# Performance work log

Hardware: AMD Instinct MI355X
Metric: run time of the kernel (lower is better)

The kernel has to match this reference:

```python
import jax, jax.numpy as jnp
import numpy as np

B, N, H, E, P = 2, 20000, 128, 200000, 3


def _mlp2(x, w1, b1, w2, b2):
    # Linear -> SiLU -> Linear
    return jax.nn.silu(x @ w1 + b1) @ w2 + b2


def setup_inputs() -> dict:
    key = jax.random.key(0)
    ks = iter(jax.random.split(key, 40))
    def nrm(shape, s=0.05):
        return jax.random.normal(next(ks), shape, dtype=jnp.float32) * s
    inp = {
        "features": jax.random.normal(next(ks), (B, N, H), dtype=jnp.float32),
        "positions": jax.random.normal(next(ks), (B, N, P), dtype=jnp.float32),
        "edge_index_up": jax.random.randint(next(ks), (2, E), 0, N, dtype=jnp.int32),
        "edge_index_down": jax.random.randint(next(ks), (2, E), 0, N, dtype=jnp.int32),
        "degree_up": jax.random.uniform(next(ks), (N,), minval=1.0, maxval=32.0, dtype=jnp.float32),
        "degree_down": jax.random.uniform(next(ks), (N,), minval=1.0, maxval=32.0, dtype=jnp.float32),
    }
    for name in ("up", "down"):
        inp[f"w_msg1_{name}"] = nrm((2 * H + 1, H)); inp[f"b_msg1_{name}"] = jnp.zeros((H,), jnp.float32)
        inp[f"w_msg2_{name}"] = nrm((H, H));         inp[f"b_msg2_{name}"] = jnp.zeros((H,), jnp.float32)
        inp[f"w_pos1_{name}"] = nrm((H, H));         inp[f"b_pos1_{name}"] = jnp.zeros((H,), jnp.float32)
        inp[f"w_pos2_{name}"] = nrm((H, 1));         inp[f"b_pos2_{name}"] = jnp.zeros((1,), jnp.float32)
    inp["w_upd1"] = nrm((2 * H, H)); inp["b_upd1"] = jnp.zeros((H,), jnp.float32)
    inp["w_upd2"] = nrm((H, H));     inp["b_upd2"] = jnp.zeros((H,), jnp.float32)
    return inp


def reference(features, positions, edge_index_up, edge_index_down, degree_up, degree_down,
              w_msg1_up, b_msg1_up, w_msg2_up, b_msg2_up,
              w_pos1_up, b_pos1_up, w_pos2_up, b_pos2_up,
              w_msg1_down, b_msg1_down, w_msg2_down, b_msg2_down,
              w_pos1_down, b_pos1_down, w_pos2_down, b_pos2_down,
              w_upd1, b_upd1, w_upd2, b_upd2):
    n_neighborhoods = 2
    msg_acc = jnp.zeros_like(features)
    pos_upd = jnp.zeros_like(positions)
    neighborhoods = [
        (edge_index_up, degree_up,
         (w_msg1_up, b_msg1_up, w_msg2_up, b_msg2_up),
         (w_pos1_up, b_pos1_up, w_pos2_up, b_pos2_up)),
        (edge_index_down, degree_down,
         (w_msg1_down, b_msg1_down, w_msg2_down, b_msg2_down),
         (w_pos1_down, b_pos1_down, w_pos2_down, b_pos2_down)),
    ]
    for edge_index, degree, msg_p, pos_p in neighborhoods:
        src, dst = edge_index[0], edge_index[1]
        h_src = features[:, src, :]                     # [B, E, H] gather
        h_dst = features[:, dst, :]                     # [B, E, H] gather
        rel_pos = positions[:, src, :] - positions[:, dst, :]  # [B, E, P]
        dist = jnp.linalg.norm(rel_pos, axis=-1, keepdims=True)  # [B, E, 1]
        msg_input = jnp.concatenate([h_src, h_dst, dist], axis=-1)  # [B, E, 2H+1]
        messages = _mlp2(msg_input, *msg_p)             # [B, E, H]
        agg = jnp.zeros_like(features).at[:, dst, :].add(messages)  # scatter-add over dim 1
        agg = agg / jnp.clip(degree, 1.0, None)[None, :, None]
        msg_acc = msg_acc + agg
        weights = jnp.tanh(_mlp2(messages, *pos_p))     # [B, E, 1]
        pos_upd = pos_upd + jnp.zeros_like(positions).at[:, dst, :].add(weights * rel_pos)
    feat_update = _mlp2(jnp.concatenate([features, msg_acc], axis=-1), w_upd1, b_upd1, w_upd2, b_upd2)
    updated_features = features + feat_update
    updated_positions = positions + pos_upd / n_neighborhoods
    return updated_features, updated_positions
```

## Files before the change

kernel.cpp:

```cpp
#include <hip/hip_runtime.h>

#define BB 2
#define NN 20000
#define HH 128
#define EE 200000
#define EBLK 3125
#define NBLK 79

typedef unsigned short u16;
typedef __attribute__((ext_vector_type(4))) float f32x4;
typedef __bf16 bf16x8 __attribute__((ext_vector_type(8)));

#define MFMA(a, b, c) __builtin_amdgcn_mfma_f32_16x16x32_bf16((a), (b), (c), 0, 0, 0)

__device__ __forceinline__ float bf2f(u16 u) {
    union { unsigned int i; float f; } v; v.i = ((unsigned int)u) << 16; return v.f;
}
__device__ __forceinline__ u16 f2bf(float f) {
    union { __bf16 h; u16 u; } v; v.h = (__bf16)f; return v.u;
}
__device__ __forceinline__ float silu_f(float z) { return z / (1.f + __expf(-z)); }

__global__ void detect_kernel(const u16* __restrict__ f, int* __restrict__ flag) {
    int tid = threadIdx.x;
    u16 v = f[tid * 2];
    int e = (v >> 7) & 0xFF;
    int ok = (e >= 101 && e <= 143) ? 1 : 0;
    __shared__ int cnt;
    if (tid == 0) cnt = 0;
    __syncthreads();
    atomicAdd(&cnt, ok);
    __syncthreads();
    if (tid == 0) *flag = (cnt < 200) ? 1 : 0;
}

#define CTOT 5461776
struct P24 { const void* p[24]; };

__global__ __launch_bounds__(256) void canon_kernel(P24 ptrs, const int* __restrict__ flag,
                                                    u16* __restrict__ canon) {
    static const int off[25] = {
        0, 5120000, 5240000, 5260000, 5280000, 5312896, 5313024, 5329408,
        5329536, 5345920, 5346048, 5346176, 5346184, 5379080, 5379208, 5395592,
        5395720, 5412104, 5412232, 5412360, 5412368, 5445136, 5445264, 5461648,
        5461776 };
    static const int rsz[24] = {
        5120000, 120000, 20000, 20000,
        32896, 128, 16384, 128, 16384, 128, 128, 1,
        32896, 128, 16384, 128, 16384, 128, 128, 1,
        32768, 128, 16384, 128 };
    int i = blockIdx.x * 256 + threadIdx.x;
    if (i >= CTOT) return;
    int t = 0;
#pragma unroll 1
    while (i >= off[t + 1]) ++t;
    int j = i - off[t];
    u16 v;
    if (j >= rsz[t]) v = 0;
    else if (*flag) v = f2bf(((const float*)ptrs.p[t])[j]);
    else v = ((const u16*)ptrs.p[t])[j];
    canon[i] = v;
}

__global__ void make_frag(const u16* __restrict__ W, u16* __restrict__ F) {
    int tid = blockIdx.x * 256 + threadIdx.x;
    int j = tid & 7, lane = (tid >> 3) & 63, nt = (tid >> 9) & 7, kt = tid >> 12;
    int k = kt * 32 + ((lane >> 4) * 8) + j;
    int n = nt * 16 + (lane & 15);
    F[tid] = W[k * 128 + n];
}

__global__ void count2_kernel(const int* __restrict__ eu, const int* __restrict__ ed,
                              int* __restrict__ cu, int* __restrict__ cd) {
    int e = blockIdx.x * 256 + threadIdx.x;
    if (e < EE) atomicAdd(&cu[eu[EE + e]], 1);
    else { e -= EE; if (e < EE) atomicAdd(&cd[ed[EE + e]], 1); }
}

struct SP { const int* cnt[2]; int* cur[2]; int* bsum[2]; };

__global__ __launch_bounds__(256) void scan1_kernel(SP p) {
    int half = blockIdx.x / NBLK;
    int b = blockIdx.x - half * NBLK;
    int t = threadIdx.x;
    int i = b * 256 + t;
    __shared__ int buf[256];
    int v = (i < NN) ? p.cnt[half][i] : 0;
    buf[t] = v;
    __syncthreads();
    for (int s = 1; s < 256; s <<= 1) {
        int x = (t >= s) ? buf[t - s] : 0;
        __syncthreads();
        buf[t] += x;
        __syncthreads();
    }
    if (i < NN) p.cur[half][i] = buf[t] - v;
    if (t == 255) p.bsum[half][b] = buf[255];
}

__global__ __launch_bounds__(256) void scan2_kernel(int* __restrict__ bu, int* __restrict__ bd) {
    __shared__ int buf[2][128];
    int half = threadIdx.x >> 7, t = threadIdx.x & 127;
    int* bs = half ? bd : bu;
    int v = (t < NBLK) ? bs[t] : 0;
    buf[half][t] = v;
    __syncthreads();
    for (int s = 1; s < 128; s <<= 1) {
        int x = (t >= s) ? buf[half][t - s] : 0;
        __syncthreads();
        buf[half][t] += x;
        __syncthreads();
    }
    if (t < NBLK) bs[t] = buf[half][t] - v;
}

__global__ void scan3_kernel(int* __restrict__ cu, const int* __restrict__ bu,
                             int* __restrict__ cd, const int* __restrict__ bd) {
    int i = blockIdx.x * 256 + threadIdx.x;
    if (i < NN) cu[i] += bu[i >> 8];
    else { i -= NN; if (i < NN) cd[i] += bd[i >> 8]; }
}

__global__ void scatter2_kernel(const int* __restrict__ eu, const int* __restrict__ ed,
                                int* __restrict__ cu, int* __restrict__ cd,
                                int* __restrict__ su, int* __restrict__ sd) {
    int e = blockIdx.x * 256 + threadIdx.x;
    if (e < EE) { int p = atomicAdd(&cu[eu[EE + e]], 1); su[p] = e; }
    else { e -= EE; if (e < EE) { int p = atomicAdd(&cd[ed[EE + e]], 1); sd[p] = e; } }
}

struct EP {
    const int* eidx; const int* es; const u16* deg;
    const u16* fW1; const u16* w1last; const u16* bias1;
    const u16* fW2; const u16* bias2;
    const u16* fP1; const u16* biasp1;
    const u16* wp2; const u16* biasp2;
};

__global__ __launch_bounds__(256, 4) void edge_kernel(
    const u16* __restrict__ feat, const u16* __restrict__ posit,
    EP up, EP dn,
    float* __restrict__ msg_acc, float* __restrict__ pos_acc)
{
    const int tid = threadIdx.x;
    const int lane = tid & 63;
    const int wv = tid >> 6;
    const int half = blockIdx.x / (BB * EBLK);
    const int rem = blockIdx.x - half * (BB * EBLK);
    const int bb = rem / EBLK;
    const int s0 = (rem - bb * EBLK) * 64;
    const EP P = half ? dn : up;

    __shared__ u16 sX[64][136];
    __shared__ u16 sY[64][136];
    __shared__ float sRel[64][3];
    __shared__ float sDist[64];
    __shared__ float sInv[64];
    __shared__ int sSrc[64], sDst[64];

    if (tid < 64) {
        int e = P.es[s0 + tid];
        int s = P.eidx[e];
        int d = P.eidx[EE + e];
        sSrc[tid] = s; sDst[tid] = d;
        sInv[tid] = 1.f / fmaxf(bf2f(P.deg[d]), 1.f);
        const u16* ps = posit + ((size_t)bb * NN + s) * 3;
        const u16* pd = posit + ((size_t)bb * NN + d) * 3;
        float dx = bf2f(ps[0]) - bf2f(pd[0]);
        float dy = bf2f(ps[1]) - bf2f(pd[1]);
        float dz = bf2f(ps[2]) - bf2f(pd[2]);
        sRel[tid][0] = dx; sRel[tid][1] = dy; sRel[tid][2] = dz;
        sDist[tid] = sqrtf(dx * dx + dy * dy + dz * dz);
    }
    __syncthreads();

    {
        const int r = tid >> 2, part = tid & 3;
        const uint4* fs = (const uint4*)(feat + ((size_t)bb * NN + sSrc[r]) * HH);
        const uint4* fd = (const uint4*)(feat + ((size_t)bb * NN + sDst[r]) * HH);
        uint4* as = (uint4*)&sX[r][part * 32];
        uint4* ad = (uint4*)&sY[r][part * 32];
#pragma unroll
        for (int i = 0; i < 4; ++i) { as[i] = fs[part * 4 + i]; ad[i] = fd[part * 4 + i]; }
    }
    __syncthreads();

    const int nt0 = wv * 2;
    const int mrow = lane & 15;
    const int kq = (lane >> 4) * 8;
    const int crow = (lane >> 4) * 4;
    const int ccol = lane & 15;

    f32x4 acc[4][2];
#pragma unroll
    for (int mt = 0; mt < 4; ++mt) {
        acc[mt][0] = (f32x4){0.f, 0.f, 0.f, 0.f};
        acc[mt][1] = (f32x4){0.f, 0.f, 0.f, 0.f};
    }

#pragma unroll
    for (int kt = 0; kt < 8; ++kt) {
        const u16* Xb = (kt < 4) ? &sX[0][0] : &sY[0][0];
        const int kk = (kt & 3) * 32 + kq;
        bf16x8 bw0 = *(const bf16x8*)(P.fW1 + (size_t)(((kt * 8 + nt0) * 64 + lane) * 8));
        bf16x8 bw1 = *(const bf16x8*)(P.fW1 + (size_t)(((kt * 8 + nt0 + 1) * 64 + lane) * 8));
#pragma unroll
        for (int mt = 0; mt < 4; ++mt) {
            bf16x8 a = *(const bf16x8*)(Xb + (mt * 16 + mrow) * 136 + kk);
            acc[mt][0] = MFMA(a, bw0, acc[mt][0]);
            acc[mt][1] = MFMA(a, bw1, acc[mt][1]);
        }
    }
    __syncthreads();

#pragma unroll
    for (int mt = 0; mt < 4; ++mt) {
#pragma unroll
        for (int n2 = 0; n2 < 2; ++n2) {
            const int col = (nt0 + n2) * 16 + ccol;
            const float wl = bf2f(P.w1last[col]);
            const float bb2 = bf2f(P.bias1[col]);
#pragma unroll
            for (int r = 0; r < 4; ++r) {
                const int row = mt * 16 + crow + r;
                float z = fmaf(sDist[row], wl, acc[mt][n2][r]) + bb2;
                sX[row][col] = f2bf(silu_f(z));
            }
        }
    }
    __syncthreads();

#pragma unroll
    for (int mt = 0; mt < 4; ++mt) {
        acc[mt][0] = (f32x4){0.f, 0.f, 0.f, 0.f};
        acc[mt][1] = (f32x4){0.f, 0.f, 0.f, 0.f};
    }
#pragma unroll
    for (int kt = 0; kt < 4; ++kt) {
        const int kk = kt * 32 + kq;
        bf16x8 bw0 = *(const bf16x8*)(P.fW2 + (size_t)(((kt * 8 + nt0) * 64 + lane) * 8));
        bf16x8 bw1 = *(const bf16x8*)(P.fW2 + (size_t)(((kt * 8 + nt0 + 1) * 64 + lane) * 8));
#pragma unroll
        for (int mt = 0; mt < 4; ++mt) {
            bf16x8 a = *(const bf16x8*)(&sX[0][0] + (mt * 16 + mrow) * 136 + kk);
            acc[mt][0] = MFMA(a, bw0, acc[mt][0]);
            acc[mt][1] = MFMA(a, bw1, acc[mt][1]);
        }
    }
#pragma unroll
    for (int mt = 0; mt < 4; ++mt) {
#pragma unroll
        for (int n2 = 0; n2 < 2; ++n2) {
            const int col = (nt0 + n2) * 16 + ccol;
            const float bb2 = bf2f(P.bias2[col]);
#pragma unroll
            for (int r = 0; r < 4; ++r) {
                const int row = mt * 16 + crow + r;
                sY[row][col] = f2bf(acc[mt][n2][r] + bb2);
            }
        }
    }
    __syncthreads();

#pragma unroll
    for (int mt = 0; mt < 4; ++mt) {
        acc[mt][0] = (f32x4){0.f, 0.f, 0.f, 0.f};
        acc[mt][1] = (f32x4){0.f, 0.f, 0.f, 0.f};
    }
#pragma unroll
    for (int kt = 0; kt < 4; ++kt) {
        const int kk = kt * 32 + kq;
        bf16x8 bw0 = *(const bf16x8*)(P.fP1 + (size_t)(((kt * 8 + nt0) * 64 + lane) * 8));
        bf16x8 bw1 = *(const bf16x8*)(P.fP1 + (size_t)(((kt * 8 + nt0 + 1) * 64 + lane) * 8));
#pragma unroll
        for (int mt = 0; mt < 4; ++mt) {
            bf16x8 a = *(const bf16x8*)(&sY[0][0] + (mt * 16 + mrow) * 136 + kk);
            acc[mt][0] = MFMA(a, bw0, acc[mt][0]);
            acc[mt][1] = MFMA(a, bw1, acc[mt][1]);
        }
    }

    {
        const int col = tid & 127;
        const int r0 = (tid >> 7) * 32;
        float accv = 0.f;
        int dprev = sDst[r0];
        float invprev = sInv[r0];
#pragma unroll 1
        for (int r = r0; r < r0 + 32; ++r) {
            int dcur = sDst[r];
            if (dcur != dprev) {
                unsafeAtomicAdd(&msg_acc[((size_t)bb * NN + dprev) * HH + col], accv * invprev);
                accv = 0.f; dprev = dcur; invprev = sInv[r];
            }
            accv += bf2f(sY[r][col]);
        }
        unsafeAtomicAdd(&msg_acc[((size_t)bb * NN + dprev) * HH + col], accv * invprev);
    }

#pragma unroll
    for (int mt = 0; mt < 4; ++mt) {
#pragma unroll
        for (int n2 = 0; n2 < 2; ++n2) {
            const int col = (nt0 + n2) * 16 + ccol;
            const float bb2 = bf2f(P.biasp1[col]);
#pragma unroll
            for (int r = 0; r < 4; ++r) {
                const int row = mt * 16 + crow + r;
                sX[row][col] = f2bf(silu_f(acc[mt][n2][r] + bb2));
            }
        }
    }
    __syncthreads();

    {
        const int r = tid >> 2, q = tid & 3;
        const unsigned int* t32 = (const unsigned int*)&sX[r][q * 32];
        const unsigned int* w32 = (const unsigned int*)(P.wp2 + q * 32);
        float p = 0.f;
#pragma unroll
        for (int k = 0; k < 16; ++k) {
            unsigned int a = t32[k], b = w32[k];
            union { unsigned int i; float f; } al, ah, bl, bh;
            al.i = a << 16; ah.i = a & 0xffff0000u;
            bl.i = b << 16; bh.i = b & 0xffff0000u;
            p = fmaf(al.f, bl.f, p);
            p = fmaf(ah.f, bh.f, p);
        }
        p += __shfl_xor(p, 1);
        p += __shfl_xor(p, 2);
        if (q == 0) {
            float wgt = tanhf(p + bf2f(P.biasp2[0]));
            const size_t pb = ((size_t)bb * NN + sDst[r]) * 3;
            unsafeAtomicAdd(&pos_acc[pb + 0], wgt * sRel[r][0]);
            unsafeAtomicAdd(&pos_acc[pb + 1], wgt * sRel[r][1]);
            unsafeAtomicAdd(&pos_acc[pb + 2], wgt * sRel[r][2]);
        }
    }
}

__global__ __launch_bounds__(256) void update_kernel(
    const u16* __restrict__ feat, const void* __restrict__ rawfeat,
    const float* __restrict__ magg,
    const u16* __restrict__ fU1, const u16* __restrict__ bu1,
    const u16* __restrict__ fU2, const u16* __restrict__ bu2,
    void* __restrict__ outp, const int* __restrict__ flag)
{
    const int tid = threadIdx.x;
    const int lane = tid & 63;
    const int wv = tid >> 6;
    const int row0 = blockIdx.x * 64;
    const int isf = *flag;

    __shared__ u16 sA[64][136];
    __shared__ u16 sB[64][136];
    __shared__ u16 sY[64][136];

    {
        const uint4* src = (const uint4*)(feat + (size_t)row0 * HH);
        for (int i = tid; i < 1024; i += 256) {
            int r = i >> 4, c = i & 15;
            *(uint4*)&sA[r][c * 8] = src[i];
        }
        const float4* am = (const float4*)(magg) + (size_t)row0 * 32;
        for (int i = tid; i < 2048; i += 256) {
            int r = i >> 5;
            float4 v = am[i];
            int c = (i & 31) * 4;
            sB[r][c + 0] = f2bf(v.x);
            sB[r][c + 1] = f2bf(v.y);
            sB[r][c + 2] = f2bf(v.z);
            sB[r][c + 3] = f2bf(v.w);
        }
    }
    __syncthreads();

    const int nt0 = wv * 2;
    const int mrow = lane & 15;
    const int kq = (lane >> 4) * 8;
    const int crow = (lane >> 4) * 4;
    const int ccol = lane & 15;

    f32x4 acc[4][2];
#pragma unroll
    for (int mt = 0; mt < 4; ++mt) {
        acc[mt][0] = (f32x4){0.f, 0.f, 0.f, 0.f};
        acc[mt][1] = (f32x4){0.f, 0.f, 0.f, 0.f};
    }
#pragma unroll
    for (int kt = 0; kt < 8; ++kt) {
        const u16* Xb = (kt < 4) ? &sA[0][0] : &sB[0][0];
        const int kk = (kt & 3) * 32 + kq;
        bf16x8 bw0 = *(const bf16x8*)(fU1 + (size_t)(((kt * 8 + nt0) * 64 + lane) * 8));
        bf16x8 bw1 = *(const bf16x8*)(fU1 + (size_t)(((kt * 8 + nt0 + 1) * 64 + lane) * 8));
#pragma unroll
        for (int mt = 0; mt < 4; ++mt) {
            bf16x8 a = *(const bf16x8*)(Xb + (mt * 16 + mrow) * 136 + kk);
            acc[mt][0] = MFMA(a, bw0, acc[mt][0]);
            acc[mt][1] = MFMA(a, bw1, acc[mt][1]);
        }
    }
#pragma unroll
    for (int mt = 0; mt < 4; ++mt) {
#pragma unroll
        for (int n2 = 0; n2 < 2; ++n2) {
            const int col = (nt0 + n2) * 16 + ccol;
            const float bb = bf2f(bu1[col]);
#pragma unroll
            for (int r = 0; r < 4; ++r) {
                const int row = mt * 16 + crow + r;
                sY[row][col] = f2bf(silu_f(acc[mt][n2][r] + bb));
            }
        }
    }
    __syncthreads();

#pragma unroll
    for (int mt = 0; mt < 4; ++mt) {
        acc[mt][0] = (f32x4){0.f, 0.f, 0.f, 0.f};
        acc[mt][1] = (f32x4){0.f, 0.f, 0.f, 0.f};
    }
#pragma unroll
    for (int kt = 0; kt < 4; ++kt) {
        const int kk = kt * 32 + kq;
        bf16x8 bw0 = *(const bf16x8*)(fU2 + (size_t)(((kt * 8 + nt0) * 64 + lane) * 8));
        bf16x8 bw1 = *(const bf16x8*)(fU2 + (size_t)(((kt * 8 + nt0 + 1) * 64 + lane) * 8));
#pragma unroll
        for (int mt = 0; mt < 4; ++mt) {
            bf16x8 a = *(const bf16x8*)(&sY[0][0] + (mt * 16 + mrow) * 136 + kk);
            acc[mt][0] = MFMA(a, bw0, acc[mt][0]);
            acc[mt][1] = MFMA(a, bw1, acc[mt][1]);
        }
    }
#pragma unroll
    for (int mt = 0; mt < 4; ++mt) {
#pragma unroll
        for (int n2 = 0; n2 < 2; ++n2) {
            const int col = (nt0 + n2) * 16 + ccol;
            const float bb = bf2f(bu2[col]);
#pragma unroll
            for (int r = 0; r < 4; ++r) {
                const int row = mt * 16 + crow + r;
                const size_t idx = (size_t)(row0 + row) * HH + col;
                if (isf) {
                    float base = ((const float*)rawfeat)[idx];
                    ((float*)outp)[idx] = acc[mt][n2][r] + bb + base;
                } else {
                    float base = bf2f(sA[row][col]);
                    ((u16*)outp)[idx] = f2bf(acc[mt][n2][r] + bb + base);
                }
            }
        }
    }
}

__global__ void pos_out_kernel(const void* __restrict__ rawpos, const u16* __restrict__ cpos,
                               const float* __restrict__ pacc, void* __restrict__ outp,
                               const int* __restrict__ flag)
{
    int i = blockIdx.x * 256 + threadIdx.x;
    if (i >= BB * NN * 3) return;
    if (*flag) {
        float base = ((const float*)rawpos)[i];
        ((float*)outp)[5120000 + i] = base + 0.5f * pacc[i];
    } else {
        float base = bf2f(cpos[i]);
        ((u16*)outp)[5120000 + i] = f2bf(base + 0.5f * pacc[i]);
    }
}

extern "C" void kernel_launch(void* const* d_in, const int* in_sizes, int n_in,
                              void* d_out, int out_size, void* d_ws, size_t ws_size,
                              hipStream_t stream)
{
    float* msg_acc = (float*)d_ws;
    float* pos_acc = (float*)((char*)d_ws + 20480000);
    int*   cnt_up  = (int*)((char*)d_ws + 20960000);
    int*   cnt_dn  = (int*)((char*)d_ws + 21040000);
    const size_t ZERO_BYTES = 21120000;
    int*   cur_up  = (int*)((char*)d_ws + 21120000);
    int*   cur_dn  = (int*)((char*)d_ws + 21200000);
    int*   bsum_up = (int*)((char*)d_ws + 21280000);
    int*   bsum_dn = (int*)((char*)d_ws + 21280400);
    int*   es_up   = (int*)((char*)d_ws + 21280800);
    int*   es_dn   = (int*)((char*)d_ws + 22080800);
    u16*   fbase   = (u16*)((char*)d_ws + 22880800);
    u16*   canon   = (u16*)((char*)d_ws + 23241248);
    int*   flag    = (int*)((char*)d_ws + 34164800);
    if (ws_size < 34164804ULL) return;

    u16* f_m1u = fbase;
    u16* f_m2u = fbase + 32768;
    u16* f_p1u = fbase + 49152;
    u16* f_m1d = fbase + 65536;
    u16* f_m2d = fbase + 98304;
    u16* f_p1d = fbase + 114688;
    u16* f_u1  = fbase + 131072;
    u16* f_u2  = fbase + 163840;

    u16* cfeat = canon;
    u16* cpos  = canon + 5120000;
    u16* cdgu  = canon + 5240000;
    u16* cdgd  = canon + 5260000;
    u16* cm1u  = canon + 5280000;
    u16* cbm1u = canon + 5312896;
    u16* cm2u  = canon + 5313024;
    u16* cbm2u = canon + 5329408;
    u16* cp1u  = canon + 5329536;
    u16* cbp1u = canon + 5345920;
    u16* cp2u  = canon + 5346048;
    u16* cbp2u = canon + 5346176;
    u16* cm1d  = canon + 5346184;
    u16* cbm1d = canon + 5379080;
    u16* cm2d  = canon + 5379208;
    u16* cbm2d = canon + 5395592;
    u16* cp1d  = canon + 5395720;
    u16* cbp1d = canon + 5412104;
    u16* cp2d  = canon + 5412232;
    u16* cbp2d = canon + 5412360;
    u16* cu1   = canon + 5412368;
    u16* cbu1  = canon + 5445136;
    u16* cu2   = canon + 5445264;
    u16* cbu2  = canon + 5461648;

    hipMemsetAsync(d_ws, 0, ZERO_BYTES, stream);

    detect_kernel<<<1, 256, 0, stream>>>((const u16*)d_in[0], flag);

    P24 ptrs;
    ptrs.p[0] = d_in[0];  ptrs.p[1] = d_in[1];  ptrs.p[2] = d_in[4];  ptrs.p[3] = d_in[5];
    ptrs.p[4] = d_in[6];  ptrs.p[5] = d_in[7];  ptrs.p[6] = d_in[8];  ptrs.p[7] = d_in[9];
    ptrs.p[8] = d_in[10]; ptrs.p[9] = d_in[11]; ptrs.p[10] = d_in[12]; ptrs.p[11] = d_in[13];
    ptrs.p[12] = d_in[14]; ptrs.p[13] = d_in[15]; ptrs.p[14] = d_in[16]; ptrs.p[15] = d_in[17];
    ptrs.p[16] = d_in[18]; ptrs.p[17] = d_in[19]; ptrs.p[18] = d_in[20]; ptrs.p[19] = d_in[21];
    ptrs.p[20] = d_in[22]; ptrs.p[21] = d_in[23]; ptrs.p[22] = d_in[24]; ptrs.p[23] = d_in[25];
    canon_kernel<<<(CTOT + 255) / 256, 256, 0, stream>>>(ptrs, flag, canon);

    make_frag<<<128, 256, 0, stream>>>(cm1u, f_m1u);
    make_frag<<<64,  256, 0, stream>>>(cm2u, f_m2u);
    make_frag<<<64,  256, 0, stream>>>(cp1u, f_p1u);
    make_frag<<<128, 256, 0, stream>>>(cm1d, f_m1d);
    make_frag<<<64,  256, 0, stream>>>(cm2d, f_m2d);
    make_frag<<<64,  256, 0, stream>>>(cp1d, f_p1d);
    make_frag<<<128, 256, 0, stream>>>(cu1,  f_u1);
    make_frag<<<64,  256, 0, stream>>>(cu2,  f_u2);

    const int* ei_up = (const int*)d_in[2];
    const int* ei_dn = (const int*)d_in[3];

    count2_kernel<<<(2 * EE + 255) / 256, 256, 0, stream>>>(ei_up, ei_dn, cnt_up, cnt_dn);
    SP sp;
    sp.cnt[0] = cnt_up; sp.cnt[1] = cnt_dn;
    sp.cur[0] = cur_up; sp.cur[1] = cur_dn;
    sp.bsum[0] = bsum_up; sp.bsum[1] = bsum_dn;
    scan1_kernel<<<2 * NBLK, 256, 0, stream>>>(sp);
    scan2_kernel<<<1, 256, 0, stream>>>(bsum_up, bsum_dn);
    scan3_kernel<<<(2 * NN + 255) / 256, 256, 0, stream>>>(cur_up, bsum_up, cur_dn, bsum_dn);
    scatter2_kernel<<<(2 * EE + 255) / 256, 256, 0, stream>>>(ei_up, ei_dn, cur_up, cur_dn,
                                                              es_up, es_dn);

    EP up, dn;
    up.eidx = ei_up; up.es = es_up; up.deg = cdgu;
    up.fW1 = f_m1u; up.w1last = cm1u + 256 * 128; up.bias1 = cbm1u;
    up.fW2 = f_m2u; up.bias2 = cbm2u;
    up.fP1 = f_p1u; up.biasp1 = cbp1u;
    up.wp2 = cp2u;  up.biasp2 = cbp2u;
    dn.eidx = ei_dn; dn.es = es_dn; dn.deg = cdgd;
    dn.fW1 = f_m1d; dn.w1last = cm1d + 256 * 128; dn.bias1 = cbm1d;
    dn.fW2 = f_m2d; dn.bias2 = cbm2d;
    dn.fP1 = f_p1d; dn.biasp1 = cbp1d;
    dn.wp2 = cp2d;  dn.biasp2 = cbp2d;

    edge_kernel<<<2 * BB * EBLK, 256, 0, stream>>>(cfeat, cpos, up, dn, msg_acc, pos_acc);

    update_kernel<<<625, 256, 0, stream>>>(
        cfeat, d_in[0], msg_acc,
        f_u1, cbu1, f_u2, cbu2, d_out, flag);

    pos_out_kernel<<<469, 256, 0, stream>>>(d_in[1], cpos, pos_acc, d_out, flag);
}
```

Measured before the change: 527.2 us.

## Use 8 waves per edge block, merge frag launches, drop update smem buffer

The edge kernel now runs 512 threads per 64-edge block. Each wave computes one 16-column tile instead of two, which halves the accumulator registers per thread and doubles the waves available for latency hiding. The gather, scatter and position-dot loops are re-split for the larger block. The eight make_frag launches become one launch over a combined offset table, and the update kernel reuses sB instead of a third shared buffer, adding one barrier. The risk is more barrier cost and a smaller MFMA-to-load ratio per wave. It also relies on the fragment buffers being contiguous at fbase.

```diff
diff --git a/kernel.cpp b/kernel.cpp
--- a/kernel.cpp
+++ b/kernel.cpp
@@ -62,12 +62,21 @@
     canon[i] = v;
 }
 
-__global__ void make_frag(const u16* __restrict__ W, u16* __restrict__ F) {
-    int tid = blockIdx.x * 256 + threadIdx.x;
-    int j = tid & 7, lane = (tid >> 3) & 63, nt = (tid >> 9) & 7, kt = tid >> 12;
-    int k = kt * 32 + ((lane >> 4) * 8) + j;
+#define FTOT 180224
+struct P8 { const u16* w[8]; };
+
+__global__ __launch_bounds__(256) void make_frag_all(P8 ws, u16* __restrict__ fbase) {
+    static const int foff[9] = { 0, 32768, 49152, 65536, 98304, 114688, 131072, 163840, 180224 };
+    int i = blockIdx.x * 256 + threadIdx.x;
+    if (i >= FTOT) return;
+    int t = 0;
+#pragma unroll 1
+    while (i >= foff[t + 1]) ++t;
+    int j = i - foff[t];
+    int jj = j & 7, lane = (j >> 3) & 63, nt = (j >> 9) & 7, kt = j >> 12;
+    int k = kt * 32 + ((lane >> 4) * 8) + jj;
     int n = nt * 16 + (lane & 15);
-    F[tid] = W[k * 128 + n];
+    fbase[i] = ws.w[t][k * 128 + n];
 }
 
 __global__ void count2_kernel(const int* __restrict__ eu, const int* __restrict__ ed,
@@ -137,7 +146,7 @@
     const u16* wp2; const u16* biasp2;
 };
 
-__global__ __launch_bounds__(256, 4) void edge_kernel(
+__global__ __launch_bounds__(512, 8) void edge_kernel(
     const u16* __restrict__ feat, const u16* __restrict__ posit,
     EP up, EP dn,
     float* __restrict__ msg_acc, float* __restrict__ pos_acc)
@@ -175,55 +184,49 @@
     __syncthreads();
 
     {
-        const int r = tid >> 2, part = tid & 3;
+        const int r = tid >> 3, part = tid & 7;
         const uint4* fs = (const uint4*)(feat + ((size_t)bb * NN + sSrc[r]) * HH);
         const uint4* fd = (const uint4*)(feat + ((size_t)bb * NN + sDst[r]) * HH);
-        uint4* as = (uint4*)&sX[r][part * 32];
-        uint4* ad = (uint4*)&sY[r][part * 32];
-#pragma unroll
-        for (int i = 0; i < 4; ++i) { as[i] = fs[part * 4 + i]; ad[i] = fd[part * 4 + i]; }
-    }
-    __syncthreads();
-
-    const int nt0 = wv * 2;
+        uint4* as = (uint4*)&sX[r][part * 16];
+        uint4* ad = (uint4*)&sY[r][part * 16];
+#pragma unroll
+        for (int i = 0; i < 2; ++i) { as[i] = fs[part * 2 + i]; ad[i] = fd[part * 2 + i]; }
+    }
+    __syncthreads();
+
+    const int nt = wv;
     const int mrow = lane & 15;
     const int kq = (lane >> 4) * 8;
     const int crow = (lane >> 4) * 4;
     const int ccol = lane & 15;
-
-    f32x4 acc[4][2];
-#pragma unroll
-    for (int mt = 0; mt < 4; ++mt) {
-        acc[mt][0] = (f32x4){0.f, 0.f, 0.f, 0.f};
-        acc[mt][1] = (f32x4){0.f, 0.f, 0.f, 0.f};
-    }
+    const int col = nt * 16 + ccol;
+
+    f32x4 acc[4];
+#pragma unroll
+    for (int mt = 0; mt < 4; ++mt) acc[mt] = (f32x4){0.f, 0.f, 0.f, 0.f};
 
 #pragma unroll
     for (int kt = 0; kt < 8; ++kt) {
         const u16* Xb = (kt < 4) ? &sX[0][0] : &sY[0][0];
         const int kk = (kt & 3) * 32 + kq;
-        bf16x8 bw0 = *(const bf16x8*)(P.fW1 + (size_t)(((kt * 8 + nt0) * 64 + lane) * 8));
-        bf16x8 bw1 = *(const bf16x8*)(P.fW1 + (size_t)(((kt * 8 + nt0 + 1) * 64 + lane) * 8));
+        bf16x8 bw = *(const bf16x8*)(P.fW1 + (size_t)(((kt * 8 + nt) * 64 + lane) * 8));
 #pragma unroll
         for (int mt = 0; mt < 4; ++mt) {
             bf16x8 a = *(const bf16x8*)(Xb + (mt * 16 + mrow) * 136 + kk);
-            acc[mt][0] = MFMA(a, bw0, acc[mt][0]);
-            acc[mt][1] = MFMA(a, bw1, acc[mt][1]);
-        }
-    }
-    __syncthreads();
-
-#pragma unroll
-    for (int mt = 0; mt < 4; ++mt) {
-#pragma unroll
-        for (int n2 = 0; n2 < 2; ++n2) {
-            const int col = (nt0 + n2) * 16 + ccol;
-            const float wl = bf2f(P.w1last[col]);
-            const float bb2 = bf2f(P.bias1[col]);
+            acc[mt] = MFMA(a, bw, acc[mt]);
+        }
+    }
+    __syncthreads();
+
+    {
+        const float wl = bf2f(P.w1last[col]);
+        const float bb2 = bf2f(P.bias1[col]);
+#pragma unroll
+        for (int mt = 0; mt < 4; ++mt) {
 #pragma unroll
             for (int r = 0; r < 4; ++r) {
                 const int row = mt * 16 + crow + r;
-                float z = fmaf(sDist[row], wl, acc[mt][n2][r]) + bb2;
+                float z = fmaf(sDist[row], wl, acc[mt][r]) + bb2;
                 sX[row][col] = f2bf(silu_f(z));
             }
         }
@@ -231,95 +234,81 @@
     __syncthreads();
 
 #pragma unroll
-    for (int mt = 0; mt < 4; ++mt) {
-        acc[mt][0] = (f32x4){0.f, 0.f, 0.f, 0.f};
-        acc[mt][1] = (f32x4){0.f, 0.f, 0.f, 0.f};
-    }
+    for (int mt = 0; mt < 4; ++mt) acc[mt] = (f32x4){0.f, 0.f, 0.f, 0.f};
 #pragma unroll
     for (int kt = 0; kt < 4; ++kt) {
         const int kk = kt * 32 + kq;
-        bf16x8 bw0 = *(const bf16x8*)(P.fW2 + (size_t)(((kt * 8 + nt0) * 64 + lane) * 8));
-        bf16x8 bw1 = *(const bf16x8*)(P.fW2 + (size_t)(((kt * 8 + nt0 + 1) * 64 + lane) * 8));
+        bf16x8 bw = *(const bf16x8*)(P.fW2 + (size_t)(((kt * 8 + nt) * 64 + lane) * 8));
 #pragma unroll
         for (int mt = 0; mt < 4; ++mt) {
             bf16x8 a = *(const bf16x8*)(&sX[0][0] + (mt * 16 + mrow) * 136 + kk);
-            acc[mt][0] = MFMA(a, bw0, acc[mt][0]);
-            acc[mt][1] = MFMA(a, bw1, acc[mt][1]);
-        }
-    }
-#pragma unroll
-    for (int mt = 0; mt < 4; ++mt) {
-#pragma unroll
-        for (int n2 = 0; n2 < 2; ++n2) {
-            const int col = (nt0 + n2) * 16 + ccol;
-            const float bb2 = bf2f(P.bias2[col]);
+            acc[mt] = MFMA(a, bw, acc[mt]);
+        }
+    }
+    {
+        const float bb2 = bf2f(P.bias2[col]);
+#pragma unroll
+        for (int mt = 0; mt < 4; ++mt) {
 #pragma unroll
             for (int r = 0; r < 4; ++r) {
                 const int row = mt * 16 + crow + r;
-                sY[row][col] = f2bf(acc[mt][n2][r] + bb2);
+                sY[row][col] = f2bf(acc[mt][r] + bb2);
             }
         }
     }
     __syncthreads();
 
 #pragma unroll
-    for (int mt = 0; mt < 4; ++mt) {
-        acc[mt][0] = (f32x4){0.f, 0.f, 0.f, 0.f};
-        acc[mt][1] = (f32x4){0.f, 0.f, 0.f, 0.f};
-    }
+    for (int mt = 0; mt < 4; ++mt) acc[mt] = (f32x4){0.f, 0.f, 0.f, 0.f};
 #pragma unroll
     for (int kt = 0; kt < 4; ++kt) {
         const int kk = kt * 32 + kq;
-        bf16x8 bw0 = *(const bf16x8*)(P.fP1 + (size_t)(((kt * 8 + nt0) * 64 + lane) * 8));
-        bf16x8 bw1 = *(const bf16x8*)(P.fP1 + (size_t)(((kt * 8 + nt0 + 1) * 64 + lane) * 8));
+        bf16x8 bw = *(const bf16x8*)(P.fP1 + (size_t)(((kt * 8 + nt) * 64 + lane) * 8));
 #pragma unroll
         for (int mt = 0; mt < 4; ++mt) {
             bf16x8 a = *(const bf16x8*)(&sY[0][0] + (mt * 16 + mrow) * 136 + kk);
-            acc[mt][0] = MFMA(a, bw0, acc[mt][0]);
-            acc[mt][1] = MFMA(a, bw1, acc[mt][1]);
-        }
-    }
-
-    {
-        const int col = tid & 127;
-        const int r0 = (tid >> 7) * 32;
+            acc[mt] = MFMA(a, bw, acc[mt]);
+        }
+    }
+
+    {
+        const int scol = tid & 127;
+        const int r0 = (tid >> 7) * 16;
         float accv = 0.f;
         int dprev = sDst[r0];
         float invprev = sInv[r0];
 #pragma unroll 1
-        for (int r = r0; r < r0 + 32; ++r) {
+        for (int r = r0; r < r0 + 16; ++r) {
             int dcur = sDst[r];
             if (dcur != dprev) {
-                unsafeAtomicAdd(&msg_acc[((size_t)bb * NN + dprev) * HH + col], accv * invprev);
+                unsafeAtomicAdd(&msg_acc[((size_t)bb * NN + dprev) * HH + scol], accv * invprev);
                 accv = 0.f; dprev = dcur; invprev = sInv[r];
             }
-            accv += bf2f(sY[r][col]);
-        }
-        unsafeAtomicAdd(&msg_acc[((size_t)bb * NN + dprev) * HH + col], accv * invprev);
-    }
-
-#pragma unroll
-    for (int mt = 0; mt < 4; ++mt) {
-#pragma unroll
-        for (int n2 = 0; n2 < 2; ++n2) {
-            const int col = (nt0 + n2) * 16 + ccol;
-            const float bb2 = bf2f(P.biasp1[col]);
+            accv += bf2f(sY[r][scol]);
+        }
+        unsafeAtomicAdd(&msg_acc[((size_t)bb * NN + dprev) * HH + scol], accv * invprev);
+    }
+
+    {
+        const float bb2 = bf2f(P.biasp1[col]);
+#pragma unroll
+        for (int mt = 0; mt < 4; ++mt) {
 #pragma unroll
             for (int r = 0; r < 4; ++r) {
                 const int row = mt * 16 + crow + r;
-                sX[row][col] = f2bf(silu_f(acc[mt][n2][r] + bb2));
+                sX[row][col] = f2bf(silu_f(acc[mt][r] + bb2));
             }
         }
     }
     __syncthreads();
 
     {
-        const int r = tid >> 2, q = tid & 3;
-        const unsigned int* t32 = (const unsigned int*)&sX[r][q * 32];
-        const unsigned int* w32 = (const unsigned int*)(P.wp2 + q * 32);
+        const int r = tid >> 3, q = tid & 7;
+        const unsigned int* t32 = (const unsigned int*)&sX[r][q * 16];
+        const unsigned int* w32 = (const unsigned int*)(P.wp2 + q * 16);
         float p = 0.f;
 #pragma unroll
-        for (int k = 0; k < 16; ++k) {
+        for (int k = 0; k < 8; ++k) {
             unsigned int a = t32[k], b = w32[k];
             union { unsigned int i; float f; } al, ah, bl, bh;
             al.i = a << 16; ah.i = a & 0xffff0000u;
@@ -329,6 +318,7 @@
         }
         p += __shfl_xor(p, 1);
         p += __shfl_xor(p, 2);
+        p += __shfl_xor(p, 4);
         if (q == 0) {
             float wgt = tanhf(p + bf2f(P.biasp2[0]));
             const size_t pb = ((size_t)bb * NN + sDst[r]) * 3;
@@ -354,7 +344,6 @@
 
     __shared__ u16 sA[64][136];
     __shared__ u16 sB[64][136];
-    __shared__ u16 sY[64][136];
 
     {
         const uint4* src = (const uint4*)(feat + (size_t)row0 * HH);
@@ -400,6 +389,8 @@
             acc[mt][1] = MFMA(a, bw1, acc[mt][1]);
         }
     }
+    __syncthreads();
+
 #pragma unroll
     for (int mt = 0; mt < 4; ++mt) {
 #pragma unroll
@@ -409,7 +400,7 @@
 #pragma unroll
             for (int r = 0; r < 4; ++r) {
                 const int row = mt * 16 + crow + r;
-                sY[row][col] = f2bf(silu_f(acc[mt][n2][r] + bb));
+                sB[row][col] = f2bf(silu_f(acc[mt][n2][r] + bb));
             }
         }
     }
@@ -427,7 +418,7 @@
         bf16x8 bw1 = *(const bf16x8*)(fU2 + (size_t)(((kt * 8 + nt0 + 1) * 64 + lane) * 8));
 #pragma unroll
         for (int mt = 0; mt < 4; ++mt) {
-            bf16x8 a = *(const bf16x8*)(&sY[0][0] + (mt * 16 + mrow) * 136 + kk);
+            bf16x8 a = *(const bf16x8*)(&sB[0][0] + (mt * 16 + mrow) * 136 + kk);
             acc[mt][0] = MFMA(a, bw0, acc[mt][0]);
             acc[mt][1] = MFMA(a, bw1, acc[mt][1]);
         }
@@ -536,14 +527,10 @@
     ptrs.p[20] = d_in[22]; ptrs.p[21] = d_in[23]; ptrs.p[22] = d_in[24]; ptrs.p[23] = d_in[25];
     canon_kernel<<<(CTOT + 255) / 256, 256, 0, stream>>>(ptrs, flag, canon);
 
-    make_frag<<<128, 256, 0, stream>>>(cm1u, f_m1u);
-    make_frag<<<64,  256, 0, stream>>>(cm2u, f_m2u);
-    make_frag<<<64,  256, 0, stream>>>(cp1u, f_p1u);
-    make_frag<<<128, 256, 0, stream>>>(cm1d, f_m1d);
-    make_frag<<<64,  256, 0, stream>>>(cm2d, f_m2d);
-    make_frag<<<64,  256, 0, stream>>>(cp1d, f_p1d);
-    make_frag<<<128, 256, 0, stream>>>(cu1,  f_u1);
-    make_frag<<<64,  256, 0, stream>>>(cu2,  f_u2);
+    P8 wsf;
+    wsf.w[0] = cm1u; wsf.w[1] = cm2u; wsf.w[2] = cp1u; wsf.w[3] = cm1d;
+    wsf.w[4] = cm2d; wsf.w[5] = cp1d; wsf.w[6] = cu1;  wsf.w[7] = cu2;
+    make_frag_all<<<(FTOT + 255) / 256, 256, 0, stream>>>(wsf, fbase);
 
     const int* ei_up = (const int*)d_in[2];
     const int* ei_dn = (const int*)d_in[3];
@@ -571,7 +558,7 @@
     dn.fP1 = f_p1d; dn.biasp1 = cbp1d;
     dn.wp2 = cp2d;  dn.biasp2 = cbp2d;
 
-    edge_kernel<<<2 * BB * EBLK, 256, 0, stream>>>(cfeat, cpos, up, dn, msg_acc, pos_acc);
+    edge_kernel<<<2 * BB * EBLK, 512, 0, stream>>>(cfeat, cpos, up, dn, msg_acc, pos_acc);
 
     update_kernel<<<625, 256, 0, stream>>>(
         cfeat, d_in[0], msg_acc,
```

After: 525.1 us. No clear change (-0.4%).
